# Kernel tuning notes

Hardware: AMD Instinct MI355X
Metric: run time of the kernel (lower is better)

Reference implementation:

```python
import jax, jax.numpy as jnp
import numpy as np

# Llama-2-7B-like GQA attention, prefill over packed equal-length sequences
H = 4096      # hidden_size
NH = 32       # num_attention_heads
NKV = 8       # num_key_value_heads
HD = H // NH  # head_dim = 128
B = 4         # number of packed sequences
S = 1024      # seq_len per sequence
T = B * S     # total packed tokens
BASE = 10000.0  # rope_theta


def setup_inputs() -> dict:
    key = jax.random.key(0)
    ks = jax.random.split(key, 5)
    x = jax.random.normal(ks[0], (T, H), jnp.float32)
    positions = jnp.tile(jnp.arange(S, dtype=jnp.int32), B)  # per-seq positions
    kv_cache = jnp.zeros((1,), jnp.float32)  # placeholder (prefill: kv from current tokens)
    init = 0.02
    wq = jax.random.normal(ks[1], (NH * HD, H), jnp.float32) * init
    wk = jax.random.normal(ks[2], (NKV * HD, H), jnp.float32) * init
    wv = jax.random.normal(ks[3], (NKV * HD, H), jnp.float32) * init
    wo = jax.random.normal(ks[4], (H, NH * HD), jnp.float32) * init
    return {"x": x, "positions": positions, "kv_cache": kv_cache,
            "wq": wq, "wk": wk, "wv": wv, "wo": wo, "seq_len": S}


def _rope(xh, cos_b, sin_b):
    # xh: [T, Hh, D]; cos_b/sin_b: [T, 1, D] (freqs repeat-interleaved by 2)
    half = xh.shape[-1] // 2
    x_rot = jnp.concatenate([-xh[..., half:], xh[..., :half]], axis=-1)
    return xh * cos_b + x_rot * sin_b


def reference(x, positions, kv_cache, wq, wk, wv, wo, seq_len):
    Tn = x.shape[0]
    q = (x @ wq.T).reshape(Tn, NH, HD)
    k = (x @ wk.T).reshape(Tn, NKV, HD)
    v = (x @ wv.T).reshape(Tn, NKV, HD)
    # GQA: repeat_interleave kv heads
    rep = NH // NKV
    k = jnp.repeat(k, rep, axis=1)
    v = jnp.repeat(v, rep, axis=1)
    # RoPE tables (faithful to _precompute_freqs/_rotary_embeddings)
    inv_freq = 1.0 / (BASE ** (jnp.arange(0, HD, 2, dtype=jnp.float32) / HD))
    t = jnp.arange(seq_len, dtype=jnp.float32)
    freqs = t[:, None] * inv_freq[None, :]            # [S, D/2]
    cos, sin = jnp.cos(freqs), jnp.sin(freqs)
    pos = jnp.clip(positions.astype(jnp.int32), 0, seq_len - 1)
    cos_b = jnp.repeat(cos[pos], 2, axis=-1)[:, None, :]  # [T,1,D]
    sin_b = jnp.repeat(sin[pos], 2, axis=-1)[:, None, :]
    q = _rope(q, cos_b, sin_b)
    k = _rope(k, cos_b, sin_b)
    # Paged attention (prefill): causal attention within each packed sequence
    Bn = Tn // seq_len
    qb = q.reshape(Bn, seq_len, NH, HD)
    kb = k.reshape(Bn, seq_len, NH, HD)
    vb = v.reshape(Bn, seq_len, NH, HD)
    scores = jnp.einsum('bqhd,bkhd->bhqk', qb, kb) * (HD ** -0.5)
    causal = jnp.tril(jnp.ones((seq_len, seq_len), bool))
    scores = jnp.where(causal[None, None], scores, -jnp.inf)
    probs = jax.nn.softmax(scores, axis=-1)
    out = jnp.einsum('bhqk,bkhd->bqhd', probs, vb).reshape(Tn, NH * HD)
    return out @ wo.T
```

## Files before the change

### kernel.cpp

```cpp
#include <hip/hip_runtime.h>
#include <hip/hip_bf16.h>
#include <math.h>

#define T_TOK 4096
#define HID   4096
#define NHQ   32
#define NKVH  8
#define HDIM  128
#define SEQ   1024
#define NBATCH 4

typedef __attribute__((ext_vector_type(8))) short bf16x8;
typedef __attribute__((ext_vector_type(4))) float f32x4;

__device__ __forceinline__ unsigned short f2bf(float f) {
  union { float f; unsigned int u; } x; x.f = f;
  unsigned int r = x.u + 0x7FFFu + ((x.u >> 16) & 1u);
  return (unsigned short)(r >> 16);
}

#define GLOAD_LDS16(gp, lp)                                                        \
  __builtin_amdgcn_global_load_lds(                                                \
      (__attribute__((address_space(1))) void*)(unsigned long long)(const void*)(gp), \
      (__attribute__((address_space(3))) void*)(unsigned long long)(const void*)(lp), \
      16, 0, 0)

__global__ __launch_bounds__(256) void cast_all_k(const float* __restrict__ x,
                                                  const float* __restrict__ wq,
                                                  const float* __restrict__ wk,
                                                  const float* __restrict__ wv,
                                                  const float* __restrict__ wo,
                                                  unsigned short* __restrict__ xb,
                                                  unsigned short* __restrict__ wqkv,
                                                  unsigned short* __restrict__ wob) {
  int i = blockIdx.x * 256 + threadIdx.x;
  const float* src; unsigned short* dst; int off;
  if (i < 4194304)       { src = x;  dst = xb;   off = i; }
  else if (i < 8388608)  { src = wq; dst = wqkv; off = i - 4194304; }
  else if (i < 9437184)  { src = wk; dst = wqkv + 16777216; off = i - 8388608; }
  else if (i < 10485760) { src = wv; dst = wqkv + 20971520; off = i - 9437184; }
  else                   { src = wo; dst = wob;  off = i - 10485760; }
  float4 f = ((const float4*)src)[off];
  ushort4 o;
  o.x = f2bf(f.x); o.y = f2bf(f.y); o.z = f2bf(f.z); o.w = f2bf(f.w);
  ((ushort4*)dst)[off] = o;
}

__global__ __launch_bounds__(512, 2) void gemm_qkv(const unsigned short* __restrict__ A,
                                                   const unsigned short* __restrict__ B,
                                                   const int* __restrict__ pos,
                                                   unsigned short* __restrict__ qr,
                                                   unsigned short* __restrict__ kr,
                                                   unsigned short* __restrict__ vbuf) {
  const int K = 4096, nt = 64;
  __shared__ unsigned short AS[3][16384];
  __shared__ unsigned short BS[3][8192];
  const int tid  = threadIdx.x;
  const int lane = tid & 63;
  const int wave = tid >> 6;
  const int m16  = lane & 15;
  const int quad = lane >> 4;
  const int wm   = wave >> 1;
  const int wn   = wave & 1;

  const int gx = 48;
  const int orig = blockIdx.y * gx + blockIdx.x;
  const int swz = (orig & 7) * 96 + (orig >> 3);
  const long rowBase = (long)(swz / gx) * 256;
  const long colBase = (long)(swz % gx) * 128;

  int aoff[2], boff[2];
#pragma unroll
  for (int ks = 0; ks < 2; ++ks) {
    int sx = ((ks * 4 + quad) ^ (m16 & 7)) * 8;
    aoff[ks] = (wm * 64 + m16) * 64 + sx;
    boff[ks] = (wn * 32 + m16) * 64 + sx;
  }

  const long Kl = K;
  const int sck = ((tid & 7) ^ ((tid >> 3) & 7)) * 8;
  const unsigned short* gA = A + (rowBase + (tid >> 3)) * Kl + sck;
  const unsigned short* gB = B + (colBase + (tid >> 3)) * Kl + sck;
  const int dofs = wave * 512;

#define STG_B(slot_, ko_) { GLOAD_LDS16(gB + (ko_),            &BS[slot_][dofs]);         \
                            GLOAD_LDS16(gB + (ko_) + 64 * Kl,  &BS[slot_][4096 + dofs]); }
#define STG_A(slot_, ko_) { GLOAD_LDS16(gA + (ko_),            &AS[slot_][dofs]);         \
                            GLOAD_LDS16(gA + (ko_) + 64 * Kl,  &AS[slot_][4096 + dofs]);  \
                            GLOAD_LDS16(gA + (ko_) + 128 * Kl, &AS[slot_][8192 + dofs]);  \
                            GLOAD_LDS16(gA + (ko_) + 192 * Kl, &AS[slot_][12288 + dofs]); }

  f32x4 acc[4][4] = {};

  STG_A(0, 0); STG_B(0, 0);
  STG_A(1, 64); STG_B(1, 64);
  asm volatile("s_waitcnt vmcnt(6)" ::: "memory");
  __builtin_amdgcn_s_barrier();

  for (int g = 0; g < 22; ++g) {
#pragma unroll
    for (int u = 0; u < 3; ++u) {
      const int t = g * 3 + u;
      if (t < nt) {
        const bool doStage = (t + 2) < nt;
        const long kn = (long)(t + 2) * 64;
        bf16x8 af[4], bfr[4];

#pragma unroll
        for (int mf = 0; mf < 4; ++mf)
          af[mf] = *(const bf16x8*)(&AS[u][aoff[0] + mf * 1024]);
#pragma unroll
        for (int nf = 0; nf < 4; ++nf)
          bfr[nf] = *(const bf16x8*)(&BS[u][boff[0] + (nf & 1) * 1024 + (nf >> 1) * 4096]);
        if (doStage) STG_A((u + 2) % 3, kn);
        __builtin_amdgcn_s_barrier();
        asm volatile("s_waitcnt lgkmcnt(0)" ::: "memory");
        __builtin_amdgcn_s_setprio(1);
#pragma unroll
        for (int mf = 0; mf < 4; ++mf)
#pragma unroll
          for (int nf = 0; nf < 4; ++nf)
            acc[mf][nf] = __builtin_amdgcn_mfma_f32_16x16x32_bf16(af[mf], bfr[nf], acc[mf][nf], 0, 0, 0);
        __builtin_amdgcn_s_setprio(0);
        __builtin_amdgcn_s_barrier();

#pragma unroll
        for (int mf = 0; mf < 4; ++mf)
          af[mf] = *(const bf16x8*)(&AS[u][aoff[1] + mf * 1024]);
#pragma unroll
        for (int nf = 0; nf < 4; ++nf)
          bfr[nf] = *(const bf16x8*)(&BS[u][boff[1] + (nf & 1) * 1024 + (nf >> 1) * 4096]);
        if (doStage) STG_B((u + 2) % 3, kn);
        __builtin_amdgcn_s_barrier();
        asm volatile("s_waitcnt lgkmcnt(0)" ::: "memory");
        __builtin_amdgcn_s_setprio(1);
#pragma unroll
        for (int mf = 0; mf < 4; ++mf)
#pragma unroll
          for (int nf = 0; nf < 4; ++nf)
            acc[mf][nf] = __builtin_amdgcn_mfma_f32_16x16x32_bf16(af[mf], bfr[nf], acc[mf][nf], 0, 0, 0);
        __builtin_amdgcn_s_setprio(0);
        if (doStage)         asm volatile("s_waitcnt vmcnt(6)" ::: "memory");
        else if (t + 1 < nt) asm volatile("s_waitcnt vmcnt(0)" ::: "memory");
        __builtin_amdgcn_s_barrier();
      }
    }
  }

  const int n0 = (int)colBase;
  unsigned short* dst;
  int rstride, colofs;
  bool dorope;
  if (n0 < 4096)       { dst = qr;   rstride = NHQ * HDIM;  colofs = n0;        dorope = true; }
  else if (n0 < 5120)  { dst = kr;   rstride = NKVH * HDIM; colofs = n0 - 4096; dorope = true; }
  else                 { dst = vbuf; rstride = NKVH * HDIM; colofs = n0 - 5120; dorope = false; }
  const float c0 = -13.287712379549449f / 64.0f;
  float fA[2], fB[2];
#pragma unroll
  for (int e = 0; e < 2; ++e) {
    int d = wn * 32 + e * 16 + m16;
    fA[e] = exp2f(c0 * (float)(d >> 1));
    fB[e] = exp2f(c0 * (float)((d >> 1) + 32));
  }
#pragma unroll
  for (int mf = 0; mf < 4; ++mf) {
#pragma unroll
    for (int reg = 0; reg < 4; ++reg) {
      int grow = (int)rowBase + wm * 64 + mf * 16 + quad * 4 + reg;
      unsigned short* drow = dst + (long)grow * rstride + colofs;
      if (dorope) {
        int p = pos[grow];
        p = p < 0 ? 0 : (p > SEQ - 1 ? SEQ - 1 : p);
        float pf = (float)p;
#pragma unroll
        for (int e = 0; e < 2; ++e) {
          int d = wn * 32 + e * 16 + m16;
          float lo = acc[mf][e][reg], hi = acc[mf][e + 2][reg];
          float s1, cc1, s2, cc2;
          __sincosf(pf * fA[e], &s1, &cc1);
          __sincosf(pf * fB[e], &s2, &cc2);
          drow[d]      = f2bf(lo * cc1 - hi * s1);
          drow[d + 64] = f2bf(hi * cc2 + lo * s2);
        }
      } else {
#pragma unroll
        for (int e = 0; e < 2; ++e) {
          int d = wn * 32 + e * 16 + m16;
          drow[d]      = f2bf(acc[mf][e][reg]);
          drow[d + 64] = f2bf(acc[mf][e + 2][reg]);
        }
      }
    }
  }
}

__global__ __launch_bounds__(512, 1) void gemm_o8(const unsigned short* __restrict__ A,
                                                  const unsigned short* __restrict__ B,
                                                  float* __restrict__ C) {
  const int K = 4096, nt = 64, N = 4096;
  __shared__ unsigned short AS[2][2][128][64];
  __shared__ unsigned short BS[2][2][128][64];
  const int tid  = threadIdx.x;
  const int lane = tid & 63;
  const int wave = tid >> 6;
  const int m16  = lane & 15;
  const int quad = lane >> 4;
  const int wm2  = wave >> 2;
  const int wn2  = wave & 3;

  const int gx = 16;
  const int nwg = 256;
  const int orig = blockIdx.y * gx + blockIdx.x;
  const int swz = (orig & 7) * (nwg >> 3) + (orig >> 3);
  const long rowBase = (long)(swz / gx) * 256;
  const long colBase = (long)(swz % gx) * 256;

  int aof[2], bof[2];
#pragma unroll
  for (int ks = 0; ks < 2; ++ks) {
    int sx = ((ks * 4 + quad) ^ (m16 & 7)) * 8;
    aof[ks] = (wm2 * 64 + m16) * 64 + sx;
    bof[ks] = (wn2 * 16 + m16) * 64 + sx;
  }

  const long Kl = K;
  const int sck = ((tid & 7) ^ ((tid >> 3) & 7)) * 8;
  const unsigned short* gA = A + (rowBase + (tid >> 3)) * Kl + sck;
  const unsigned short* gB = B + (colBase + (tid >> 3)) * Kl + sck;
  const int dofs = wave * 512;

#define STGO(XS_, gX_, db_, hf_, ko_) {                                                      \
    GLOAD_LDS16(gX_ + (long)((hf_) * 128) * Kl + (ko_),      ((unsigned short*)&XS_[db_][hf_][0][0]) + dofs);  \
    GLOAD_LDS16(gX_ + (long)((hf_) * 128 + 64) * Kl + (ko_), ((unsigned short*)&XS_[db_][hf_][64][0]) + dofs); }

#define RD_A(d_, qa_) {                                                   \
    const unsigned short* Ah_ = &AS[d_][qa_][0][0];                       \
    _Pragma("unroll") for (int mf = 0; mf < 4; ++mf)                      \
      _Pragma("unroll") for (int ks = 0; ks < 2; ++ks)                    \
        af[mf][ks] = *(const bf16x8*)(Ah_ + aof[ks] + mf * 1024); }

#define RD_B(d_, qb_, dst_) {                                             \
    const unsigned short* Bh_ = &BS[d_][qb_][0][0];                       \
    _Pragma("unroll") for (int nf = 0; nf < 2; ++nf)                      \
      _Pragma("unroll") for (int ks = 0; ks < 2; ++ks)                    \
        dst_[nf][ks] = *(const bf16x8*)(Bh_ + bof[ks] + nf * 4096); }

#define MFMA16(qa_, qb_, b_) {                                            \
    _Pragma("unroll") for (int mf = 0; mf < 4; ++mf)                      \
      _Pragma("unroll") for (int nf = 0; nf < 2; ++nf)                    \
        _Pragma("unroll") for (int ks = 0; ks < 2; ++ks)                  \
          acc[qa_][qb_][mf][nf] = __builtin_amdgcn_mfma_f32_16x16x32_bf16(\
              af[mf][ks], b_[nf][ks], acc[qa_][qb_][mf][nf], 0, 0, 0); }

  f32x4 acc[2][2][4][2] = {};
  bf16x8 af[4][2], b0[2][2], b1[2][2];

  STGO(AS, gA, 0, 0, 0);   STGO(BS, gB, 0, 1, 0);
  STGO(AS, gA, 0, 1, 0);   STGO(BS, gB, 0, 0, 0);
  STGO(AS, gA, 1, 0, 64);  STGO(BS, gB, 1, 1, 64);
  STGO(AS, gA, 1, 1, 64);
  asm volatile("s_waitcnt vmcnt(6)" ::: "memory");
  __builtin_amdgcn_s_barrier();

#define KSTEP(n_, d_) {                                                               \
    RD_A(d_, 0); RD_B(d_, 0, b0);                                                     \
    if ((n_) + 1 < nt) STGO(BS, gB, (d_) ^ 1, 0, ((n_) + 1) * 64);                    \
    asm volatile("s_waitcnt lgkmcnt(8)" ::: "memory");                                \
    __builtin_amdgcn_s_barrier();                                                     \
    asm volatile("s_waitcnt lgkmcnt(0)" ::: "memory");                                \
    __builtin_amdgcn_s_setprio(1); MFMA16(0, 0, b0); __builtin_amdgcn_s_setprio(0);   \
    __builtin_amdgcn_s_barrier();                                                     \
    RD_B(d_, 1, b1);                                                                  \
    if ((n_) + 2 < nt) STGO(AS, gA, d_, 0, ((n_) + 2) * 64);                          \
    __builtin_amdgcn_s_barrier();                                                     \
    asm volatile("s_waitcnt lgkmcnt(0)" ::: "memory");                                \
    __builtin_amdgcn_s_setprio(1); MFMA16(0, 1, b1); __builtin_amdgcn_s_setprio(0);   \
    __builtin_amdgcn_s_barrier();                                                     \
    RD_A(d_, 1);                                                                      \
    if ((n_) + 2 < nt) STGO(BS, gB, d_, 1, ((n_) + 2) * 64);                          \
    __builtin_amdgcn_s_barrier();                                                     \
    asm volatile("s_waitcnt lgkmcnt(0)" ::: "memory");                                \
    __builtin_amdgcn_s_setprio(1); MFMA16(1, 1, b1); __builtin_amdgcn_s_setprio(0);   \
    __builtin_amdgcn_s_barrier();                                                     \
    if ((n_) + 2 < nt) STGO(AS, gA, d_, 1, ((n_) + 2) * 64);                          \
    __builtin_amdgcn_s_barrier();                                                     \
    __builtin_amdgcn_s_setprio(1); MFMA16(1, 0, b0); __builtin_amdgcn_s_setprio(0);   \
    if ((n_) + 2 < nt) asm volatile("s_waitcnt vmcnt(6)" ::: "memory");               \
    else               asm volatile("s_waitcnt vmcnt(0)" ::: "memory");               \
    __builtin_amdgcn_s_barrier(); }

  for (int it = 0; it < 32; ++it) {
    KSTEP(2 * it, 0);
    KSTEP(2 * it + 1, 1);
  }

#pragma unroll
  for (int qa = 0; qa < 2; ++qa)
#pragma unroll
    for (int qb = 0; qb < 2; ++qb)
#pragma unroll
      for (int mf = 0; mf < 4; ++mf)
#pragma unroll
        for (int nf = 0; nf < 2; ++nf) {
          long c = colBase + qb * 128 + wn2 * 16 + nf * 64 + m16;
#pragma unroll
          for (int reg = 0; reg < 4; ++reg) {
            long row = rowBase + qa * 128 + wm2 * 64 + mf * 16 + quad * 4 + reg;
            C[row * N + c] = acc[qa][qb][mf][nf][reg];
          }
        }
}

#define ATT_SCALE_L2 0.12754227022f
#define RESCALE_THR 8.0f
__global__ __launch_bounds__(512) void attn8(const unsigned short* __restrict__ Qp,
                                             const unsigned short* __restrict__ Kp,
                                             const unsigned short* __restrict__ Vp,
                                             unsigned short* __restrict__ Op) {
  const int pr = blockIdx.x, h = blockIdx.y, b = blockIdx.z;
  const int kvh = h >> 2;
  const int tid = threadIdx.x, wave = tid >> 6, lane = tid & 63;
  const int m16 = lane & 15, quad = lane >> 4;

  __shared__ unsigned short Ks[2][64][128];
  __shared__ unsigned short Vt[2][128][64];
  __shared__ unsigned short Ps[8][32][64];

  const unsigned short* Kh = Kp + (long)(b * SEQ) * (NKVH * HDIM) + kvh * HDIM;
  const unsigned short* Vh = Vp + (long)(b * SEQ) * (NKVH * HDIM) + kvh * HDIM;

#define STAGE_K8(ktv, bufp) {                                              \
    _Pragma("unroll")                                                      \
    for (int it_ = 0; it_ < 2; ++it_) {                                    \
      int c_ = it_ * 512 + tid;                                            \
      int row_ = c_ >> 4, psg_ = c_ & 15;                                  \
      int sg_ = (psg_ & 8) | ((psg_ & 7) ^ (row_ & 7));                    \
      GLOAD_LDS16(Kh + ((long)(ktv) * 64 + row_) * (NKVH * HDIM) + sg_ * 8,\
                  ((unsigned short*)(bufp)) + (it_ * 512 + wave * 64) * 8);\
    } }

#define LOAD_V8(ktv, dvv) {                                                \
    _Pragma("unroll")                                                      \
    for (int it_ = 0; it_ < 2; ++it_)                                      \
      dvv[it_] = *(const uint4*)(Vh + ((long)(ktv) * 64 + lane) * (NKVH * HDIM) + (it_ * 8 + wave) * 8); }

#define SCATTER_V8(bufp, dvv) {                                            \
    _Pragma("unroll")                                                      \
    for (int it_ = 0; it_ < 2; ++it_) {                                    \
      const unsigned short* pv_ = (const unsigned short*)&dvv[it_];        \
      int seg_ = it_ * 8 + wave;                                           \
      _Pragma("unroll")                                                    \
      for (int e_ = 0; e_ < 8; ++e_) {                                     \
        int d_ = seg_ * 8 + e_;                                            \
        (bufp)[d_][((((lane >> 3) + d_) & 7) * 8) + (lane & 7)] = pv_[e_]; \
      } } }

  for (int pass = 0; pass < 2; ++pass) {
    const int qt = pass ? pr : (3 - pr);
    const int qbase = qt * 256;
    const int wq_lo = qbase + wave * 32;

    bf16x8 qa[2][4];
#pragma unroll
    for (int i = 0; i < 2; ++i) {
      const unsigned short* qrow =
          Qp + (long)(b * SEQ + wq_lo + i * 16 + m16) * (NHQ * HDIM) + h * HDIM;
#pragma unroll
      for (int kk = 0; kk < 4; ++kk)
        qa[i][kk] = *(const bf16x8*)(qrow + kk * 32 + quad * 8);
    }

    f32x4 o[2][8] = {};
    float mrow[2][4], lrow[2][4];
#pragma unroll
    for (int i = 0; i < 2; ++i)
#pragma unroll
      for (int r = 0; r < 4; ++r) { mrow[i][r] = -1e30f; lrow[i][r] = 0.f; }

    const int nkt = (qt + 1) * 4;

    {
      STAGE_K8(0, Ks[0]);
      uint4 dv0[2];
      LOAD_V8(0, dv0);
      asm volatile("s_waitcnt vmcnt(0)" ::: "memory");
      SCATTER_V8(Vt[0], dv0);
    }
    __syncthreads();

    for (int kt = 0; kt < nkt; ++kt) {
      const int cb = kt & 1;
      const bool active = (kt * 64) <= (wq_lo + 31);
      const bool more = (kt + 1) < nkt;

      f32x4 s4[2][4] = {};
      if (active) {
        __builtin_amdgcn_s_setprio(1);
#pragma unroll
        for (int kk = 0; kk < 4; ++kk) {
          bf16x8 kbf[4];
#pragma unroll
          for (int j = 0; j < 4; ++j) {
            int row = j * 16 + m16;
            int cl = kk * 4 + quad;
            int ps = (cl & 8) | ((cl & 7) ^ (row & 7));
            kbf[j] = *(const bf16x8*)(&Ks[cb][row][ps * 8]);
          }
#pragma unroll
          for (int i = 0; i < 2; ++i)
#pragma unroll
            for (int j = 0; j < 4; ++j)
              s4[i][j] = __builtin_amdgcn_mfma_f32_16x16x32_bf16(qa[i][kk], kbf[j], s4[i][j], 0, 0, 0);
        }
        __builtin_amdgcn_s_setprio(0);
      }

      uint4 dv[2];
      if (more) {
        STAGE_K8(kt + 1, Ks[cb ^ 1]);
        LOAD_V8(kt + 1, dv);
      }
      asm volatile("" ::: "memory");

      if (active) {
        const bool full = (kt * 64 + 63) <= wq_lo;
#pragma unroll
        for (int i = 0; i < 2; ++i) {
#pragma unroll
          for (int r = 0; r < 4; ++r) {
            const int qrow = i * 16 + quad * 4 + r;
            const int qi = qbase + wave * 32 + qrow;
            float v[4];
#pragma unroll
            for (int j = 0; j < 4; ++j) {
              v[j] = s4[i][j][r] * ATT_SCALE_L2;
              if (!full && (kt * 64 + j * 16 + m16 > qi)) v[j] = -1e30f;
            }
            float mx = fmaxf(fmaxf(v[0], v[1]), fmaxf(v[2], v[3]));
            mx = fmaxf(mx, __shfl_xor(mx, 1));
            mx = fmaxf(mx, __shfl_xor(mx, 2));
            mx = fmaxf(mx, __shfl_xor(mx, 4));
            mx = fmaxf(mx, __shfl_xor(mx, 8));
            float mold = mrow[i][r];
            bool skip = (mx <= mold + RESCALE_THR);
            float mnew = skip ? mold : mx;
            float rs = 0.f;
#pragma unroll
            for (int j = 0; j < 4; ++j) {
              float pj = exp2f(v[j] - mnew);
              rs += pj;
              int col = j * 16 + m16;
              Ps[wave][qrow][((((col >> 3) + qrow) & 7) * 8) + (col & 7)] = f2bf(pj);
            }
            if (!skip) {
              float alpha = exp2f(mold - mnew);
              lrow[i][r] *= alpha;
#pragma unroll
              for (int n = 0; n < 8; ++n) o[i][n][r] *= alpha;
              mrow[i][r] = mnew;
            }
            lrow[i][r] += rs;
          }
        }
        __builtin_amdgcn_s_setprio(1);
#pragma unroll
        for (int kk = 0; kk < 2; ++kk) {
          bf16x8 pa[2], vb[8];
#pragma unroll
          for (int i = 0; i < 2; ++i) {
            int row = i * 16 + m16;
            pa[i] = *(const bf16x8*)(&Ps[wave][row][(((kk * 4 + quad) + row) & 7) * 8]);
          }
#pragma unroll
          for (int n = 0; n < 8; ++n) {
            int row = n * 16 + m16;
            vb[n] = *(const bf16x8*)(&Vt[cb][row][(((kk * 4 + quad) + row) & 7) * 8]);
          }
#pragma unroll
          for (int i = 0; i < 2; ++i)
#pragma unroll
            for (int n = 0; n < 8; ++n)
              o[i][n] = __builtin_amdgcn_mfma_f32_16x16x32_bf16(pa[i], vb[n], o[i][n], 0, 0, 0);
        }
        __builtin_amdgcn_s_setprio(0);
      }

      if (more) {
        asm volatile("s_waitcnt vmcnt(0)" ::: "memory");
        SCATTER_V8(Vt[cb ^ 1], dv);
      }
      __syncthreads();
    }

#pragma unroll
    for (int i = 0; i < 2; ++i) {
#pragma unroll
      for (int r = 0; r < 4; ++r) {
        float ls = lrow[i][r];
        ls += __shfl_xor(ls, 1); ls += __shfl_xor(ls, 2);
        ls += __shfl_xor(ls, 4); ls += __shfl_xor(ls, 8);
        float inv = 1.0f / ls;
        unsigned short* orow =
            Op + (long)(b * SEQ + wq_lo + i * 16 + quad * 4 + r) * (NHQ * HDIM) + h * HDIM;
#pragma unroll
        for (int n = 0; n < 8; ++n)
          orow[n * 16 + m16] = f2bf(o[i][n][r] * inv);
      }
    }
  }
}

extern "C" void kernel_launch(void* const* d_in, const int* in_sizes, int n_in,
                              void* d_out, int out_size, void* d_ws, size_t ws_size,
                              hipStream_t stream) {
  (void)in_sizes; (void)n_in; (void)out_size; (void)ws_size;
  const float* x  = (const float*)d_in[0];
  const int* pos  = (const int*)d_in[1];
  const float* wq = (const float*)d_in[3];
  const float* wk = (const float*)d_in[4];
  const float* wv = (const float*)d_in[5];
  const float* wo = (const float*)d_in[6];
  float* out = (float*)d_out;

  char* ws = (char*)d_ws;
  unsigned short* xb    = (unsigned short*)(ws);
  unsigned short* wqkv  = (unsigned short*)(ws + (32ll << 20));
  unsigned short* wob   = (unsigned short*)(ws + (80ll << 20));
  unsigned short* qr    = (unsigned short*)(ws + (112ll << 20));
  unsigned short* kr    = (unsigned short*)(ws + (144ll << 20));
  unsigned short* vb_   = (unsigned short*)(ws + (152ll << 20));
  unsigned short* ao    = (unsigned short*)(ws + (160ll << 20));

  cast_all_k<<<57344, 256, 0, stream>>>(x, wq, wk, wv, wo, xb, wqkv, wob);
  gemm_qkv<<<dim3(48, 16), 512, 0, stream>>>(xb, wqkv, pos, qr, kr, vb_);
  attn8<<<dim3(2, 32, 4), 512, 0, stream>>>(qr, kr, vb_, ao);
  gemm_o8<<<dim3(16, 16), 512, 0, stream>>>(ao, wob, out);
}
```

Before: 657.1 us.

## Shrink attention query tile to 16 rows per wave and double grid

Each wave now handles 16 query rows instead of 32, so a block covers 128 queries, and the grid doubles to 512 blocks while keeping paired causal passes for load balance. V is now single-buffered in shared memory, the P buffer is halved, and launch bounds request 4 blocks per CU, all to cut registers and LDS and raise occupancy and parallelism. The cost is an extra __syncthreads per key tile before the V scatter, and K/V tiles are re-read by twice as many blocks, with fewer MFMAs per LDS load of K and V.

```diff
diff --git a/kernel.cpp b/kernel.cpp
--- a/kernel.cpp
+++ b/kernel.cpp
@@ -313,18 +313,18 @@
 
 #define ATT_SCALE_L2 0.12754227022f
 #define RESCALE_THR 8.0f
-__global__ __launch_bounds__(512) void attn8(const unsigned short* __restrict__ Qp,
-                                             const unsigned short* __restrict__ Kp,
-                                             const unsigned short* __restrict__ Vp,
-                                             unsigned short* __restrict__ Op) {
+__global__ __launch_bounds__(512, 4) void attn8(const unsigned short* __restrict__ Qp,
+                                                const unsigned short* __restrict__ Kp,
+                                                const unsigned short* __restrict__ Vp,
+                                                unsigned short* __restrict__ Op) {
   const int pr = blockIdx.x, h = blockIdx.y, b = blockIdx.z;
   const int kvh = h >> 2;
   const int tid = threadIdx.x, wave = tid >> 6, lane = tid & 63;
   const int m16 = lane & 15, quad = lane >> 4;
 
   __shared__ unsigned short Ks[2][64][128];
-  __shared__ unsigned short Vt[2][128][64];
-  __shared__ unsigned short Ps[8][32][64];
+  __shared__ unsigned short Vt[128][64];
+  __shared__ unsigned short Ps[8][16][64];
 
   const unsigned short* Kh = Kp + (long)(b * SEQ) * (NKVH * HDIM) + kvh * HDIM;
   const unsigned short* Vh = Vp + (long)(b * SEQ) * (NKVH * HDIM) + kvh * HDIM;
@@ -344,7 +344,7 @@
     for (int it_ = 0; it_ < 2; ++it_)                                      \
       dvv[it_] = *(const uint4*)(Vh + ((long)(ktv) * 64 + lane) * (NKVH * HDIM) + (it_ * 8 + wave) * 8); }
 
-#define SCATTER_V8(bufp, dvv) {                                            \
+#define SCATTER_V8(dvv) {                                                  \
     _Pragma("unroll")                                                      \
     for (int it_ = 0; it_ < 2; ++it_) {                                    \
       const unsigned short* pv_ = (const unsigned short*)&dvv[it_];        \
@@ -352,48 +352,45 @@
       _Pragma("unroll")                                                    \
       for (int e_ = 0; e_ < 8; ++e_) {                                     \
         int d_ = seg_ * 8 + e_;                                            \
-        (bufp)[d_][((((lane >> 3) + d_) & 7) * 8) + (lane & 7)] = pv_[e_]; \
+        Vt[d_][((((lane >> 3) + d_) & 7) * 8) + (lane & 7)] = pv_[e_];     \
       } } }
 
   for (int pass = 0; pass < 2; ++pass) {
-    const int qt = pass ? pr : (3 - pr);
-    const int qbase = qt * 256;
-    const int wq_lo = qbase + wave * 32;
-
-    bf16x8 qa[2][4];
-#pragma unroll
-    for (int i = 0; i < 2; ++i) {
+    const int qt = pass ? pr : (7 - pr);
+    const int qbase = qt * 128;
+    const int wq_lo = qbase + wave * 16;
+
+    bf16x8 qa[4];
+    {
       const unsigned short* qrow =
-          Qp + (long)(b * SEQ + wq_lo + i * 16 + m16) * (NHQ * HDIM) + h * HDIM;
+          Qp + (long)(b * SEQ + wq_lo + m16) * (NHQ * HDIM) + h * HDIM;
 #pragma unroll
       for (int kk = 0; kk < 4; ++kk)
-        qa[i][kk] = *(const bf16x8*)(qrow + kk * 32 + quad * 8);
+        qa[kk] = *(const bf16x8*)(qrow + kk * 32 + quad * 8);
     }
 
-    f32x4 o[2][8] = {};
-    float mrow[2][4], lrow[2][4];
-#pragma unroll
-    for (int i = 0; i < 2; ++i)
-#pragma unroll
-      for (int r = 0; r < 4; ++r) { mrow[i][r] = -1e30f; lrow[i][r] = 0.f; }
-
-    const int nkt = (qt + 1) * 4;
+    f32x4 o[8] = {};
+    float mrow[4], lrow[4];
+#pragma unroll
+    for (int r = 0; r < 4; ++r) { mrow[r] = -1e30f; lrow[r] = 0.f; }
+
+    const int nkt = qt * 2 + 2;
 
     {
       STAGE_K8(0, Ks[0]);
       uint4 dv0[2];
       LOAD_V8(0, dv0);
       asm volatile("s_waitcnt vmcnt(0)" ::: "memory");
-      SCATTER_V8(Vt[0], dv0);
+      SCATTER_V8(dv0);
     }
     __syncthreads();
 
     for (int kt = 0; kt < nkt; ++kt) {
       const int cb = kt & 1;
-      const bool active = (kt * 64) <= (wq_lo + 31);
+      const bool active = (kt * 64) <= (wq_lo + 15);
       const bool more = (kt + 1) < nkt;
 
-      f32x4 s4[2][4] = {};
+      f32x4 s4[4] = {};
       if (active) {
         __builtin_amdgcn_s_setprio(1);
 #pragma unroll
@@ -407,10 +404,8 @@
             kbf[j] = *(const bf16x8*)(&Ks[cb][row][ps * 8]);
           }
 #pragma unroll
-          for (int i = 0; i < 2; ++i)
-#pragma unroll
-            for (int j = 0; j < 4; ++j)
-              s4[i][j] = __builtin_amdgcn_mfma_f32_16x16x32_bf16(qa[i][kk], kbf[j], s4[i][j], 0, 0, 0);
+          for (int j = 0; j < 4; ++j)
+            s4[j] = __builtin_amdgcn_mfma_f32_16x16x32_bf16(qa[kk], kbf[j], s4[j], 0, 0, 0);
         }
         __builtin_amdgcn_s_setprio(0);
       }
@@ -425,87 +420,79 @@
       if (active) {
         const bool full = (kt * 64 + 63) <= wq_lo;
 #pragma unroll
-        for (int i = 0; i < 2; ++i) {
-#pragma unroll
-          for (int r = 0; r < 4; ++r) {
-            const int qrow = i * 16 + quad * 4 + r;
-            const int qi = qbase + wave * 32 + qrow;
-            float v[4];
-#pragma unroll
-            for (int j = 0; j < 4; ++j) {
-              v[j] = s4[i][j][r] * ATT_SCALE_L2;
-              if (!full && (kt * 64 + j * 16 + m16 > qi)) v[j] = -1e30f;
-            }
-            float mx = fmaxf(fmaxf(v[0], v[1]), fmaxf(v[2], v[3]));
-            mx = fmaxf(mx, __shfl_xor(mx, 1));
-            mx = fmaxf(mx, __shfl_xor(mx, 2));
-            mx = fmaxf(mx, __shfl_xor(mx, 4));
-            mx = fmaxf(mx, __shfl_xor(mx, 8));
-            float mold = mrow[i][r];
-            bool skip = (mx <= mold + RESCALE_THR);
-            float mnew = skip ? mold : mx;
-            float rs = 0.f;
-#pragma unroll
-            for (int j = 0; j < 4; ++j) {
-              float pj = exp2f(v[j] - mnew);
-              rs += pj;
-              int col = j * 16 + m16;
-              Ps[wave][qrow][((((col >> 3) + qrow) & 7) * 8) + (col & 7)] = f2bf(pj);
-            }
-            if (!skip) {
-              float alpha = exp2f(mold - mnew);
-              lrow[i][r] *= alpha;
-#pragma unroll
-              for (int n = 0; n < 8; ++n) o[i][n][r] *= alpha;
-              mrow[i][r] = mnew;
-            }
-            lrow[i][r] += rs;
-          }
+        for (int r = 0; r < 4; ++r) {
+          const int qrow = quad * 4 + r;
+          const int qi = qbase + wave * 16 + qrow;
+          float v[4];
+#pragma unroll
+          for (int j = 0; j < 4; ++j) {
+            v[j] = s4[j][r] * ATT_SCALE_L2;
+            if (!full && (kt * 64 + j * 16 + m16 > qi)) v[j] = -1e30f;
+          }
+          float mx = fmaxf(fmaxf(v[0], v[1]), fmaxf(v[2], v[3]));
+          mx = fmaxf(mx, __shfl_xor(mx, 1));
+          mx = fmaxf(mx, __shfl_xor(mx, 2));
+          mx = fmaxf(mx, __shfl_xor(mx, 4));
+          mx = fmaxf(mx, __shfl_xor(mx, 8));
+          float mold = mrow[r];
+          bool skip = (mx <= mold + RESCALE_THR);
+          float mnew = skip ? mold : mx;
+          float rs = 0.f;
+#pragma unroll
+          for (int j = 0; j < 4; ++j) {
+            float pj = exp2f(v[j] - mnew);
+            rs += pj;
+            int col = j * 16 + m16;
+            Ps[wave][qrow][((((col >> 3) + qrow) & 7) * 8) + (col & 7)] = f2bf(pj);
+          }
+          if (!skip) {
+            float alpha = exp2f(mold - mnew);
+            lrow[r] *= alpha;
+#pragma unroll
+            for (int n = 0; n < 8; ++n) o[n][r] *= alpha;
+            mrow[r] = mnew;
+          }
+          lrow[r] += rs;
         }
         __builtin_amdgcn_s_setprio(1);
 #pragma unroll
         for (int kk = 0; kk < 2; ++kk) {
-          bf16x8 pa[2], vb[8];
-#pragma unroll
-          for (int i = 0; i < 2; ++i) {
-            int row = i * 16 + m16;
-            pa[i] = *(const bf16x8*)(&Ps[wave][row][(((kk * 4 + quad) + row) & 7) * 8]);
+          bf16x8 pa, vb[8];
+          {
+            int row = m16;
+            pa = *(const bf16x8*)(&Ps[wave][row][(((kk * 4 + quad) + row) & 7) * 8]);
           }
 #pragma unroll
           for (int n = 0; n < 8; ++n) {
             int row = n * 16 + m16;
-            vb[n] = *(const bf16x8*)(&Vt[cb][row][(((kk * 4 + quad) + row) & 7) * 8]);
-          }
-#pragma unroll
-          for (int i = 0; i < 2; ++i)
-#pragma unroll
-            for (int n = 0; n < 8; ++n)
-              o[i][n] = __builtin_amdgcn_mfma_f32_16x16x32_bf16(pa[i], vb[n], o[i][n], 0, 0, 0);
+            vb[n] = *(const bf16x8*)(&Vt[row][(((kk * 4 + quad) + row) & 7) * 8]);
+          }
+#pragma unroll
+          for (int n = 0; n < 8; ++n)
+            o[n] = __builtin_amdgcn_mfma_f32_16x16x32_bf16(pa, vb[n], o[n], 0, 0, 0);
         }
         __builtin_amdgcn_s_setprio(0);
       }
 
+      __syncthreads();
       if (more) {
         asm volatile("s_waitcnt vmcnt(0)" ::: "memory");
-        SCATTER_V8(Vt[cb ^ 1], dv);
+        SCATTER_V8(dv);
       }
       __syncthreads();
     }
 
 #pragma unroll
-    for (int i = 0; i < 2; ++i) {
-#pragma unroll
-      for (int r = 0; r < 4; ++r) {
-        float ls = lrow[i][r];
-        ls += __shfl_xor(ls, 1); ls += __shfl_xor(ls, 2);
-        ls += __shfl_xor(ls, 4); ls += __shfl_xor(ls, 8);
-        float inv = 1.0f / ls;
-        unsigned short* orow =
-            Op + (long)(b * SEQ + wq_lo + i * 16 + quad * 4 + r) * (NHQ * HDIM) + h * HDIM;
-#pragma unroll
-        for (int n = 0; n < 8; ++n)
-          orow[n * 16 + m16] = f2bf(o[i][n][r] * inv);
-      }
+    for (int r = 0; r < 4; ++r) {
+      float ls = lrow[r];
+      ls += __shfl_xor(ls, 1); ls += __shfl_xor(ls, 2);
+      ls += __shfl_xor(ls, 4); ls += __shfl_xor(ls, 8);
+      float inv = 1.0f / ls;
+      unsigned short* orow =
+          Op + (long)(b * SEQ + wq_lo + quad * 4 + r) * (NHQ * HDIM) + h * HDIM;
+#pragma unroll
+      for (int n = 0; n < 8; ++n)
+        orow[n * 16 + m16] = f2bf(o[n][r] * inv);
     }
   }
 }
@@ -533,6 +520,6 @@
 
   cast_all_k<<<57344, 256, 0, stream>>>(x, wq, wk, wv, wo, xb, wqkv, wob);
   gemm_qkv<<<dim3(48, 16), 512, 0, stream>>>(xb, wqkv, pos, qr, kr, vb_);
-  attn8<<<dim3(2, 32, 4), 512, 0, stream>>>(qr, kr, vb_, ao);
+  attn8<<<dim3(4, 32, 4), 512, 0, stream>>>(qr, kr, vb_, ao);
   gemm_o8<<<dim3(16, 16), 512, 0, stream>>>(ao, wob, out);
 }
```

Result: slower. 714.4 us (+8.7%).
